# Optimization experiments

Hardware: AMD Instinct MI355X
Metric: run time of the kernel (lower is better)

Reference implementation:

```python
import jax, jax.numpy as jnp
import numpy as np

B, L, V, E, H = 256, 256, 32000, 300, 100

def _prm(key, shape, scale=0.05):
    return (jax.random.normal(key, shape) * scale).astype(jnp.float32)

def setup_inputs():
    ks = jax.random.split(jax.random.key(0), 40)
    d = {
        "p": jax.random.randint(ks[0], (B, L), 0, V),
        "q": jax.random.randint(ks[1], (B, L), 0, V),
        "embed": _prm(ks[2], (V, E), 1.0),
    }
    ins = [E, 5 * H, 7 * H, 9 * H, 11 * H]
    for i, n in enumerate(ins):
        d[f"Wih{i+1}"] = _prm(ks[3 + 2 * i], (n, 4 * H))
        d[f"Whh{i+1}"] = _prm(ks[4 + 2 * i], (H, 4 * H))
        d[f"bih{i+1}"] = jnp.zeros((4 * H,), jnp.float32)
        d[f"bhh{i+1}"] = jnp.zeros((4 * H,), jnp.float32)
    d["a1w1"] = _prm(ks[20], (9 * H, 200)); d["a1b1"] = jnp.zeros((200,), jnp.float32)
    d["a1w2"] = _prm(ks[21], (200, 9 * H)); d["a1b2"] = jnp.zeros((9 * H,), jnp.float32)
    d["a2w1"] = _prm(ks[22], (13 * H, 200)); d["a2b1"] = jnp.zeros((200,), jnp.float32)
    d["a2w2"] = _prm(ks[23], (200, 13 * H)); d["a2b2"] = jnp.zeros((13 * H,), jnp.float32)
    d["dw1"] = _prm(ks[24], (13 * H * 5, 1000)); d["db1"] = jnp.zeros((1000,), jnp.float32)
    d["dw2"] = _prm(ks[25], (1000, 1000)); d["db2"] = jnp.zeros((1000,), jnp.float32)
    d["dw3"] = _prm(ks[26], (1000, 2)); d["db3"] = jnp.zeros((2,), jnp.float32)
    return d

def _lstm_seq(x0, h0, c0, Wih, Whh, bih, bhh, n):
    # NOTE: original code feeds x[0] at EVERY timestep (source bug, kept faithful).
    pre = x0 @ Wih + bih + bhh  # [B, 4H], constant across time
    def step(carry, _):
        h, c = carry
        g = pre + h @ Whh
        i, f, gg, o = jnp.split(g, 4, axis=-1)  # torch gate order i,f,g,o
        c = jax.nn.sigmoid(f) * c + jax.nn.sigmoid(i) * jnp.tanh(gg)
        h = jax.nn.sigmoid(o) * jnp.tanh(c)
        return (h, c), h
    (h, c), hs = jax.lax.scan(step, (h0, c0), None, length=n)
    return hs, h, c  # hs: [L, B, H] time-major

def _attn(pb, qb):
    # pb, qb: [B, L, H] batch-first; per-pair cosine similarity then dual softmax
    pn = jnp.sqrt(jnp.sum(pb * pb, axis=-1))
    qn = jnp.sqrt(jnp.sum(qb * qb, axis=-1))
    dots = jnp.einsum('bih,bjh->bij', pb, qb)
    att = dots / jnp.maximum(pn[:, :, None] * qn[:, None, :], 1e-8)
    a_p = jnp.matmul(jax.nn.softmax(att, axis=2), qb)  # [B,L,H]
    a_q = jnp.matmul(jax.nn.softmax(att, axis=1), pb)  # faithful: att (not att^T) @ p, valid since Lp==Lq
    return a_p, a_q

def _ae(x, w1, b1, w2, b2):
    # dropout is identity in eval mode
    return jnp.tanh(jnp.tanh(x @ w1 + b1) @ w2 + b2)

def _forward(p, q, embed, Wih1, Whh1, bih1, bhh1, Wih2, Whh2, bih2, bhh2,
             Wih3, Whh3, bih3, bhh3, Wih4, Whh4, bih4, bhh4, Wih5, Whh5, bih5, bhh5,
             a1w1, a1b1, a1w2, a1b2, a2w1, a2b1, a2w2, a2b2,
             dw1, db1, dw2, db2, dw3, db3):
    h0 = jnp.ones((B, H), jnp.float32)
    c0 = jnp.ones((B, H), jnp.float32)
    x_p = embed[p].transpose(1, 0, 2)  # [L, B, E] time-major
    x_q = embed[q].transpose(1, 0, 2)

    def layer(x_p, x_q, Wih, Whh, bih, bhh):
        # p-loop starts fresh from (h0,c0); q-loop carries state from p-loop (faithful)
        hs_p, h, c = _lstm_seq(x_p[0], h0, c0, Wih, Whh, bih, bhh, L)
        hs_q, _, _ = _lstm_seq(x_q[0], h, c, Wih, Whh, bih, bhh, L)
        return hs_p, hs_q

    def attend_cat(hs_p, hs_q, x_p, x_q):
        a_p, a_q = _attn(hs_p.transpose(1, 0, 2), hs_q.transpose(1, 0, 2))
        xp = jnp.concatenate([hs_p, a_p.transpose(1, 0, 2), x_p], axis=2)
        xq = jnp.concatenate([hs_q, a_q.transpose(1, 0, 2), x_q], axis=2)
        return xp, xq

    h_p1, h_q1 = layer(x_p, x_q, Wih1, Whh1, bih1, bhh1)
    x_p2, x_q2 = attend_cat(h_p1, h_q1, x_p, x_q)        # [L,B,5H]
    h_p2, h_q2 = layer(x_p2, x_q2, Wih2, Whh2, bih2, bhh2)
    x_p3, x_q3 = attend_cat(h_p2, h_q2, x_p2, x_q2)      # [L,B,7H]
    h_p3, h_q3 = layer(x_p3, x_q3, Wih3, Whh3, bih3, bhh3)
    x_pe, x_qe = attend_cat(h_p3, h_q3, x_p3, x_q3)      # [L,B,9H]
    x_p4 = _ae(x_pe, a1w1, a1b1, a1w2, a1b2)
    x_q4 = _ae(x_qe, a1w1, a1b1, a1w2, a1b2)
    h_p4, h_q4 = layer(x_p4, x_q4, Wih4, Whh4, bih4, bhh4)
    x_p5, x_q5 = attend_cat(h_p4, h_q4, x_p4, x_q4)      # [L,B,11H]
    h_p5, h_q5 = layer(x_p5, x_q5, Wih5, Whh5, bih5, bhh5)
    x_pe2, x_qe2 = attend_cat(h_p5, h_q5, x_p5, x_q5)    # [L,B,13H]
    x_p_pool = _ae(x_pe2, a2w1, a2b1, a2w2, a2b2)
    x_q_pool = _ae(x_qe2, a2w1, a2b1, a2w2, a2b2)
    vp = jnp.max(x_p_pool, axis=0)  # max over time -> [B,13H]
    vq = jnp.max(x_q_pool, axis=0)
    vec = jnp.concatenate([vp, vq, vp + vq, vp - vq, jnp.abs(vp - vq)], axis=1)  # [B,65H]
    h1 = jax.nn.relu(vec @ dw1 + db1)
    h2 = jax.nn.relu(h1 @ dw2 + db2)
    return jax.nn.softmax(h2 @ dw3 + db3, axis=1)  # [B,2]

def reference(p, q, embed, Wih1, Whh1, bih1, bhh1, Wih2, Whh2, bih2, bhh2,
              Wih3, Whh3, bih3, bhh3, Wih4, Whh4, bih4, bhh4, Wih5, Whh5, bih5, bhh5,
              a1w1, a1b1, a1w2, a1b2, a2w1, a2b1, a2w2, a2b2,
              dw1, db1, dw2, db2, dw3, db3):
    return _forward(p, q, embed, Wih1, Whh1, bih1, bhh1, Wih2, Whh2, bih2, bhh2,
                    Wih3, Whh3, bih3, bhh3, Wih4, Whh4, bih4, bhh4, Wih5, Whh5, bih5, bhh5,
                    a1w1, a1b1, a1w2, a1b2, a2w1, a2b1, a2w2, a2b2,
                    dw1, db1, dw2, db2, dw3, db3)
```

## Files before the change

kernel.cpp:

```cpp
#include <hip/hip_runtime.h>
#include <hip/hip_bf16.h>
#include <cstddef>

#define NB 256
#define NL 256
#define NE 300
#define NH 100
#define NG 400
#define RT 16
#define YW 1300

typedef __hip_bfloat16 bf;
typedef __attribute__((ext_vector_type(8))) short short8v;
typedef __attribute__((ext_vector_type(4))) float float4v;

static __device__ __forceinline__ float bu2f(unsigned short u) {
  union { unsigned int i; float f; } x; x.i = ((unsigned int)u) << 16; return x.f;
}
static __device__ __forceinline__ float b2f(bf v) { return __bfloat162float(v); }
static __device__ __forceinline__ bf f2b(float f) { return __float2bfloat16(f); }
static __device__ __forceinline__ unsigned short f2bu(float f) {
  bf h = __float2bfloat16(f);
  return *reinterpret_cast<unsigned short*>(&h);
}

__global__ __launch_bounds__(256) void build_x0(
    const bf* __restrict__ segA, int dimA,
    const bf* __restrict__ segB, int dimB,
    const int* __restrict__ toks, const float* __restrict__ embed,
    float* __restrict__ X0, int in_dim, int b0)
{
  int bc = blockIdx.x;
  int tok = 0;
  if (dimA + dimB < in_dim) { tok = toks[(b0 + bc) * NL]; if (tok < 0) tok = 0; }
  for (int k = threadIdx.x; k < in_dim; k += 256) {
    float v;
    if (k < dimA) v = b2f(segA[(size_t)bc * YW + k]);
    else if (k < dimA + dimB) v = b2f(segB[(size_t)bc * YW + (k - dimA)]);
    else v = embed[(size_t)tok * NE + (k - dimA - dimB)];
    X0[(size_t)bc * in_dim + k] = v;
  }
}

__global__ __launch_bounds__(512) void lstm_kernel(
    const float* __restrict__ x0, int in_dim,
    const float* __restrict__ Wih, const float* __restrict__ Whh,
    const float* __restrict__ bih, const float* __restrict__ bhh,
    int init_ones, float* __restrict__ st,
    bf* __restrict__ hs, int hs_off, int nbc)
{
  int bc = blockIdx.x, j = threadIdx.x;
  __shared__ float g[NG];
  __shared__ __align__(16) float hb[NH];
  float wh[NH];
  float pre = 0.f;
  if (j < NG) {
    pre = bih[j] + bhh[j];
    const float4* x4 = (const float4*)(x0 + (size_t)bc * in_dim);
    for (int k4 = 0; k4 < (in_dim >> 2); k4++) {
      float4 xv = x4[k4];
      const float* wp = Wih + (size_t)(4 * k4) * NG + j;
      pre += xv.x * wp[0];
      pre += xv.y * wp[NG];
      pre += xv.z * wp[2 * NG];
      pre += xv.w * wp[3 * NG];
    }
#pragma unroll
    for (int k = 0; k < NH; k++) wh[k] = Whh[(size_t)k * NG + j];
  }
  float c = 0.f, hcur = 0.f, hprev = 0.f;
  if (j < NH) {
    if (init_ones) { hcur = 1.f; c = 1.f; }
    else { hcur = st[bc * 2 * NH + j]; c = st[bc * 2 * NH + NH + j]; }
    hb[j] = hcur;
  }
  __syncthreads();
  for (int l = 0; l < NL; l++) {
    if (j < NH && l > 0)
      hs[((size_t)(l - 1) * nbc + bc) * YW + hs_off + j] = f2b(hprev);
    if (j < NG) {
      float gs = pre;
#pragma unroll
      for (int k4 = 0; k4 < NH / 4; k4++) {
        float4 h4 = *(const float4*)&hb[4 * k4];
        gs += h4.x * wh[4 * k4] + h4.y * wh[4 * k4 + 1]
            + h4.z * wh[4 * k4 + 2] + h4.w * wh[4 * k4 + 3];
      }
      g[j] = gs;
    }
    __syncthreads();
    if (j < NH) {
      float i_g = 1.f / (1.f + expf(-g[j]));
      float f_g = 1.f / (1.f + expf(-g[NH + j]));
      float g_g = tanhf(g[2 * NH + j]);
      float o_g = 1.f / (1.f + expf(-g[3 * NH + j]));
      c = f_g * c + i_g * g_g;
      hcur = o_g * tanhf(c);
      hprev = hcur;
      hb[j] = hcur;
    }
    __syncthreads();
  }
  if (j < NH) {
    hs[((size_t)(NL - 1) * nbc + bc) * YW + hs_off + j] = f2b(hprev);
    st[bc * 2 * NH + j] = hcur;
    st[bc * 2 * NH + NH + j] = c;
  }
}

__global__ __launch_bounds__(256) void attn_scores(
    const bf* __restrict__ Pb, int hoff,
    const bf* __restrict__ Qb,
    bf* __restrict__ att, int nbc)
{
  int bc = blockIdx.y, i0 = blockIdx.x * RT, t = threadIdx.x;
  __shared__ __align__(16) float ps[NH][RT];
  __shared__ float pn[RT];
  for (int it = 0; it < 7; it++) {
    int idx = t + 256 * it;
    if (idx < NH * RT) {
      int r = idx & 15, k = idx >> 4;
      ps[k][r] = b2f(Pb[((size_t)(i0 + r) * nbc + bc) * YW + hoff + k]);
    }
  }
  __syncthreads();
  if (t < RT) {
    float s = 0.f;
    for (int k = 0; k < NH; k++) { float v = ps[k][t]; s += v * v; }
    pn[t] = sqrtf(s);
  }
  __syncthreads();
  const bf* qrow = Qb + ((size_t)t * nbc + bc) * YW + hoff;
  float dot[RT];
#pragma unroll
  for (int r = 0; r < RT; r++) dot[r] = 0.f;
  float qn = 0.f;
  for (int k = 0; k < NH; k++) {
    float qv = b2f(qrow[k]);
    qn += qv * qv;
    const float4* p4 = (const float4*)&ps[k][0];
    float4 A = p4[0], Bv = p4[1], Cv = p4[2], Dv = p4[3];
    dot[0] += A.x * qv;  dot[1] += A.y * qv;  dot[2] += A.z * qv;  dot[3] += A.w * qv;
    dot[4] += Bv.x * qv; dot[5] += Bv.y * qv; dot[6] += Bv.z * qv; dot[7] += Bv.w * qv;
    dot[8] += Cv.x * qv; dot[9] += Cv.y * qv; dot[10] += Cv.z * qv; dot[11] += Cv.w * qv;
    dot[12] += Dv.x * qv; dot[13] += Dv.y * qv; dot[14] += Dv.z * qv; dot[15] += Dv.w * qv;
  }
  float qnr = sqrtf(qn);
#pragma unroll
  for (int r = 0; r < RT; r++)
    att[((size_t)bc * NL + (i0 + r)) * NL + t] = f2b(dot[r] / fmaxf(pn[r] * qnr, 1e-8f));
}

__global__ __launch_bounds__(256) void attn_ap(
    const bf* __restrict__ att,
    const bf* __restrict__ Qb, int hoff,
    bf* __restrict__ dst, int aoff, int nbc)
{
  int bc = blockIdx.y, i0 = blockIdx.x * RT, t = threadIdx.x;
  __shared__ float w[RT][NL];
  __shared__ float inv[RT];
#pragma unroll
  for (int r = 0; r < RT; r++)
    w[r][t] = b2f(att[((size_t)bc * NL + (i0 + r)) * NL + t]);
  __syncthreads();
  {
    int r = t >> 4, s = t & 15;
    float m = -1e30f;
    for (int jj = s; jj < NL; jj += 16) m = fmaxf(m, w[r][jj]);
#pragma unroll
    for (int o = 8; o; o >>= 1) m = fmaxf(m, __shfl_xor(m, o, 16));
    float sum = 0.f;
    for (int jj = s; jj < NL; jj += 16) { float e = expf(w[r][jj] - m); w[r][jj] = e; sum += e; }
#pragma unroll
    for (int o = 8; o; o >>= 1) sum += __shfl_xor(sum, o, 16);
    if (s == 0) inv[r] = 1.f / sum;
  }
  __syncthreads();
#pragma unroll
  for (int it = 0; it < 2; it++) {
    int idx = t + 256 * it;
    if (idx >= RT * 25) break;
    int r = idx / 25, c4 = (idx % 25) * 4;
    float sc = inv[r];
    float ax = 0, ay = 0, az = 0, aw = 0;
    for (int j = 0; j < NL; j++) {
      float wv = w[r][j];
      ushort4 qv = *(const ushort4*)(Qb + ((size_t)j * nbc + bc) * YW + hoff + c4);
      ax += wv * bu2f(qv.x); ay += wv * bu2f(qv.y);
      az += wv * bu2f(qv.z); aw += wv * bu2f(qv.w);
    }
    ushort4 o4;
    o4.x = f2bu(ax * sc); o4.y = f2bu(ay * sc); o4.z = f2bu(az * sc); o4.w = f2bu(aw * sc);
    *(ushort4*)(dst + ((size_t)(i0 + r) * nbc + bc) * YW + aoff + c4) = o4;
  }
}

__global__ __launch_bounds__(256) void attn_colstats(
    const bf* __restrict__ att, float* __restrict__ cmax, float* __restrict__ csum)
{
  int bc = blockIdx.x, j = threadIdx.x;
  const bf* ab = att + (size_t)bc * NL * NL;
  float m = -1e30f;
  for (int i = 0; i < NL; i++) m = fmaxf(m, b2f(ab[(size_t)i * NL + j]));
  float s = 0.f;
  for (int i = 0; i < NL; i++) s += expf(b2f(ab[(size_t)i * NL + j]) - m);
  cmax[bc * NL + j] = m;
  csum[bc * NL + j] = s;
}

__global__ __launch_bounds__(256) void attn_aq(
    const bf* __restrict__ att, const float* __restrict__ cmax, const float* __restrict__ csum,
    const bf* __restrict__ Pb, int hoff,
    bf* __restrict__ dst, int aoff, int nbc)
{
  int bc = blockIdx.y, i0 = blockIdx.x * RT, t = threadIdx.x;
  __shared__ float w[RT][NL];
  float cm = cmax[bc * NL + t], ci = 1.f / csum[bc * NL + t];
#pragma unroll
  for (int r = 0; r < RT; r++)
    w[r][t] = expf(b2f(att[((size_t)bc * NL + (i0 + r)) * NL + t]) - cm) * ci;
  __syncthreads();
#pragma unroll
  for (int it = 0; it < 2; it++) {
    int idx = t + 256 * it;
    if (idx >= RT * 25) break;
    int r = idx / 25, c4 = (idx % 25) * 4;
    float ax = 0, ay = 0, az = 0, aw = 0;
    for (int j = 0; j < NL; j++) {
      float wv = w[r][j];
      ushort4 pv = *(const ushort4*)(Pb + ((size_t)j * nbc + bc) * YW + hoff + c4);
      ax += wv * bu2f(pv.x); ay += wv * bu2f(pv.y);
      az += wv * bu2f(pv.z); aw += wv * bu2f(pv.w);
    }
    ushort4 o4;
    o4.x = f2bu(ax); o4.y = f2bu(ay); o4.z = f2bu(az); o4.w = f2bu(aw);
    *(ushort4*)(dst + ((size_t)(i0 + r) * nbc + bc) * YW + aoff + c4) = o4;
  }
}

__global__ __launch_bounds__(256) void prep_w1T(
    const float* __restrict__ w, int K, int Kpad, short* __restrict__ dst)
{
  int col = blockIdx.y;
  int k = blockIdx.x * 256 + threadIdx.x;
  if (k < Kpad)
    dst[(size_t)col * Kpad + k] = (col < 200 && k < K) ? f2bu(w[(size_t)k * 200 + col]) : 0;
}
__global__ __launch_bounds__(256) void prep_w2T(
    const float* __restrict__ w, int N, short* __restrict__ dst)
{
  int col = blockIdx.x;
  int k = threadIdx.x;
  if (k < 224)
    dst[(size_t)col * 224 + k] = (col < N && k < 200) ? f2bu(w[(size_t)k * N + col]) : 0;
}

__global__ __launch_bounds__(256) void ae_mfma(
    const bf* __restrict__ srcA, int dimA,
    const bf* __restrict__ srcB, int dimB,
    const int* __restrict__ toks, const float* __restrict__ embed,
    int in_dim, int Kpad,
    const short* __restrict__ w1T, const float* __restrict__ b1,
    const short* __restrict__ w2T, const float* __restrict__ b2,
    int out_dim, int nch2,
    bf* __restrict__ dst, int doff,
    float* __restrict__ pmax, int pool, int nbc, int lgnbc, int b0)
{
  __shared__ short smem[24576];
  short* xsS = smem;
  short* wsS = smem + 4096;
  short* HS  = smem;
  short* w2S = smem + 17408;
  __shared__ float pmaxs[4][32];

  const int t = threadIdx.x;
  const int wave = t >> 6, lane = t & 63;
  const int lc = lane & 15;
  const int koff = (lane >> 4) << 3;

  float4v acc[13];
#pragma unroll
  for (int nt = 0; nt < 13; nt++) { acc[nt][0] = 0.f; acc[nt][1] = 0.f; acc[nt][2] = 0.f; acc[nt][3] = 0.f; }

  for (int kc = 0; kc < Kpad; kc += 64) {
    bool fastA = (kc + 64 <= dimA);
    bool fastB = (kc >= dimA) && (kc + 64 <= dimA + dimB);
    if (fastA || fastB) {
      const bf* src = fastA ? srcA : srcB;
      int coff = fastA ? kc : (kc - dimA);
      for (int idx = t; idx < 64 * 16; idx += 256) {
        int r = idx >> 4, k4 = (idx & 15) * 4;
        size_t rc = pool ? ((size_t)(blockIdx.x * 64 + r) * nbc + blockIdx.y)
                         : ((size_t)blockIdx.x * 64 + r);
        ushort4 v = *(const ushort4*)(src + rc * YW + coff + k4);
        int half = (r * 64 + k4) ^ ((r & 7) << 3);
        *(ushort4*)&xsS[half] = v;
      }
    } else {
      for (int idx = t; idx < 64 * 64; idx += 256) {
        int r = idx >> 6, kk = idx & 63;
        int k = kc + kk;
        size_t rc = pool ? ((size_t)(blockIdx.x * 64 + r) * nbc + blockIdx.y)
                         : ((size_t)blockIdx.x * 64 + r);
        unsigned short v = 0;
        if (k < dimA) v = *(const unsigned short*)&srcA[rc * YW + k];
        else if (k < dimA + dimB) v = *(const unsigned short*)&srcB[rc * YW + (k - dimA)];
        else if (k < in_dim) {
          int l = (int)(rc >> lgnbc), bb = (int)(rc & (nbc - 1));
          int tok = toks[(b0 + bb) * NL + l]; if (tok < 0) tok = 0;
          v = f2bu(embed[(size_t)tok * NE + (k - dimA - dimB)]);
        }
        xsS[(r * 64 + kk) ^ ((r & 7) << 3)] = (short)v;
      }
    }
    for (int idx = t; idx < 208 * 8; idx += 256) {
      int col = idx >> 3, k8 = (idx & 7) * 8;
      short8v v = *(const short8v*)(w1T + (size_t)col * Kpad + kc + k8);
      *(short8v*)&wsS[(col * 64 + k8) ^ ((col & 7) << 3)] = v;
    }
    __syncthreads();
    const int arow = (wave << 4) + lc;
#pragma unroll
    for (int ks = 0; ks < 2; ks++) {
      int kk = ks * 32 + koff;
      short8v a = *(const short8v*)&xsS[(arow * 64 + kk) ^ ((arow & 7) << 3)];
#pragma unroll
      for (int nt = 0; nt < 13; nt++) {
        int col = nt * 16 + lc;
        short8v b = *(const short8v*)&wsS[(col * 64 + kk) ^ ((col & 7) << 3)];
        acc[nt] = __builtin_amdgcn_mfma_f32_16x16x32_bf16(a, b, acc[nt], 0, 0, 0);
      }
    }
    __syncthreads();
  }

#pragma unroll
  for (int nt = 0; nt < 13; nt++) {
    int col = nt * 16 + lc;
    float bb = (col < 200) ? b1[col] : 0.f;
#pragma unroll
    for (int reg = 0; reg < 4; reg++) {
      int row = (wave << 4) + ((lane >> 4) << 2) + reg;
      float hv = (col < 200) ? tanhf(acc[nt][reg] + bb) : 0.f;
      HS[(row * 224 + col) ^ ((row & 7) << 3)] = (short)f2bu(hv);
    }
  }
  for (int idx = t; idx < 64 * 16; idx += 256) {
    int row = idx >> 4, col = 208 + (idx & 15);
    HS[(row * 224 + col) ^ ((row & 7) << 3)] = 0;
  }
  __syncthreads();

  for (int nc = 0; nc < nch2; nc++) {
    if (nc) __syncthreads();
    for (int idx = t; idx < 32 * 28; idx += 256) {
      int col = idx / 28, k8 = (idx % 28) * 8;
      short8v v = *(const short8v*)(w2T + (size_t)(nc * 32 + col) * 224 + k8);
      *(short8v*)&w2S[(col * 224 + k8) ^ ((col & 7) << 3)] = v;
    }
    __syncthreads();
    float4v acc2[2];
#pragma unroll
    for (int nt = 0; nt < 2; nt++) { acc2[nt][0] = 0.f; acc2[nt][1] = 0.f; acc2[nt][2] = 0.f; acc2[nt][3] = 0.f; }
    const int arow = (wave << 4) + lc;
#pragma unroll
    for (int ks = 0; ks < 7; ks++) {
      int kk = ks * 32 + koff;
      short8v a = *(const short8v*)&HS[(arow * 224 + kk) ^ ((arow & 7) << 3)];
#pragma unroll
      for (int nt = 0; nt < 2; nt++) {
        int col = nt * 16 + lc;
        short8v b = *(const short8v*)&w2S[(col * 224 + kk) ^ ((col & 7) << 3)];
        acc2[nt] = __builtin_amdgcn_mfma_f32_16x16x32_bf16(a, b, acc2[nt], 0, 0, 0);
      }
    }
    if (!pool) {
#pragma unroll
      for (int nt = 0; nt < 2; nt++) {
        int j = nc * 32 + nt * 16 + lc;
        if (j < out_dim) {
          float bb = b2[j];
#pragma unroll
          for (int reg = 0; reg < 4; reg++) {
            int row = (wave << 4) + ((lane >> 4) << 2) + reg;
            size_t rc = (size_t)blockIdx.x * 64 + row;
            dst[rc * YW + doff + j] = f2b(tanhf(acc2[nt][reg] + bb));
          }
        }
      }
    } else {
#pragma unroll
      for (int nt = 0; nt < 2; nt++) {
        int j = nc * 32 + nt * 16 + lc;
        float bb = (j < out_dim) ? b2[j] : 0.f;
        float m = -1e30f;
#pragma unroll
        for (int reg = 0; reg < 4; reg++) m = fmaxf(m, tanhf(acc2[nt][reg] + bb));
        m = fmaxf(m, __shfl_xor(m, 16));
        m = fmaxf(m, __shfl_xor(m, 32));
        if (lane < 16) pmaxs[wave][nt * 16 + lane] = m;
      }
      __syncthreads();
      if (t < 32) {
        int j = nc * 32 + t;
        if (j < out_dim) {
          float m = fmaxf(fmaxf(pmaxs[0][t], pmaxs[1][t]), fmaxf(pmaxs[2][t], pmaxs[3][t]));
          pmax[((size_t)blockIdx.x * nbc + blockIdx.y) * out_dim + j] = m;
        }
      }
    }
  }
}

__global__ __launch_bounds__(256) void pool_reduce(
    const float* __restrict__ pmax, float* __restrict__ v, int nbc, int b0)
{
  int bc = blockIdx.x;
  for (int jj = threadIdx.x; jj < 1300; jj += 256) {
    float m = -1e30f;
    for (int lc = 0; lc < 4; lc++) m = fmaxf(m, pmax[((size_t)lc * nbc + bc) * 1300 + jj]);
    v[(size_t)(b0 + bc) * 1300 + jj] = m;
  }
}

__global__ __launch_bounds__(256) void build_vec(
    const float* __restrict__ vp, const float* __restrict__ vq, float* __restrict__ vec)
{
  int b = blockIdx.x;
  float* v = vec + (size_t)b * 6500;
  for (int k = threadIdx.x; k < 1300; k += 256) {
    float a = vp[(size_t)b * 1300 + k], bq = vq[(size_t)b * 1300 + k];
    v[k] = a; v[1300 + k] = bq; v[2600 + k] = a + bq; v[3900 + k] = a - bq;
    v[5200 + k] = fabsf(a - bq);
  }
}

#define FMA16(arr, base4, wv) { \
  float4 _a = (base4)[0], _b = (base4)[1], _c = (base4)[2], _d = (base4)[3]; \
  arr[0] += _a.x * (wv); arr[1] += _a.y * (wv); arr[2] += _a.z * (wv); arr[3] += _a.w * (wv); \
  arr[4] += _b.x * (wv); arr[5] += _b.y * (wv); arr[6] += _b.z * (wv); arr[7] += _b.w * (wv); \
  arr[8] += _c.x * (wv); arr[9] += _c.y * (wv); arr[10] += _c.z * (wv); arr[11] += _c.w * (wv); \
  arr[12] += _d.x * (wv); arr[13] += _d.y * (wv); arr[14] += _d.z * (wv); arr[15] += _d.w * (wv); }

#define KT 32
#define JT 256
__global__ __launch_bounds__(256) void mlp_partial(
    const float* __restrict__ in, int K,
    const float* __restrict__ W, int N,
    float* __restrict__ part, int kslen)
{
  int rb = blockIdx.x, jb = blockIdx.y, ks = blockIdx.z;
  int t = threadIdx.x;
  int j0 = jb * JT;
  int jw = N - j0; if (jw > JT) jw = JT;
  int k0 = ks * kslen;
  int k1 = k0 + kslen; if (k1 > K) k1 = K;
  __shared__ __align__(16) float xs[KT][16];
  __shared__ __align__(16) float ws[KT][JT];
  float acc[16];
#pragma unroll
  for (int r = 0; r < 16; r++) acc[r] = 0.f;
  for (int kc = k0; kc < k1; kc += KT) {
    int klim = k1 - kc; if (klim > KT) klim = KT;
    for (int idx = t; idx < klim * 16; idx += 256) {
      int kk = idx >> 4, r = idx & 15;
      xs[kk][r] = in[(size_t)(rb * 16 + r) * K + kc + kk];
    }
    int nw4 = jw >> 2;
    for (int idx = t; idx < klim * nw4; idx += 256) {
      int kk = idx / nw4, c4 = (idx % nw4) * 4;
      *(float4*)&ws[kk][c4] =
          *(const float4*)&W[(size_t)(kc + kk) * N + j0 + c4];
    }
    __syncthreads();
    if (t < jw) {
      for (int k = 0; k < klim; k++) {
        float wv = ws[k][t];
        const float4* x4 = (const float4*)&xs[k][0];
        FMA16(acc, x4, wv);
      }
    }
    __syncthreads();
  }
  if (t < jw) {
#pragma unroll
    for (int r = 0; r < 16; r++)
      part[((size_t)blockIdx.z * NB + rb * 16 + r) * N + j0 + t] = acc[r];
  }
}

__global__ __launch_bounds__(256) void mlp_reduce(
    const float* __restrict__ part, const float* __restrict__ bias,
    float* __restrict__ out, int N, int nks)
{
  int row = blockIdx.y;
  int j = blockIdx.x * 256 + threadIdx.x;
  if (j >= N) return;
  float s = bias[j];
  for (int ks = 0; ks < nks; ks++)
    s += part[((size_t)ks * NB + row) * N + j];
  out[(size_t)row * N + j] = fmaxf(s, 0.f);
}

__global__ __launch_bounds__(64) void final_softmax(
    const float* __restrict__ h2, const float* __restrict__ dw3,
    const float* __restrict__ db3, float* __restrict__ out)
{
  int b = blockIdx.x, t = threadIdx.x;
  float a0 = 0.f, a1 = 0.f;
  for (int k = t; k < 1000; k += 64) {
    float hv = h2[(size_t)b * 1000 + k];
    a0 += hv * dw3[2 * k];
    a1 += hv * dw3[2 * k + 1];
  }
  for (int o = 32; o; o >>= 1) { a0 += __shfl_down(a0, o); a1 += __shfl_down(a1, o); }
  if (t == 0) {
    a0 += db3[0]; a1 += db3[1];
    float m = fmaxf(a0, a1);
    float e0 = expf(a0 - m), e1 = expf(a1 - m), s = e0 + e1;
    out[b * 2] = e0 / s; out[b * 2 + 1] = e1 / s;
  }
}

__global__ __launch_bounds__(256) void fill_diag(float* __restrict__ out, int n, float v)
{
  int i = blockIdx.x * 256 + threadIdx.x;
  if (i < n) out[i] = v;
}

extern "C" void kernel_launch(void* const* d_in, const int* in_sizes, int n_in,
                              void* d_out, int out_size, void* d_ws, size_t ws_size,
                              hipStream_t stream)
{
  (void)in_sizes; (void)n_in;
  const int* p = (const int*)d_in[0];
  const int* q = (const int*)d_in[1];
  const float* embed = (const float*)d_in[2];
  const float *Wih[5], *Whh[5], *bihv[5], *bhhv[5];
  for (int i = 0; i < 5; i++) {
    Wih[i] = (const float*)d_in[3 + 4 * i];
    Whh[i] = (const float*)d_in[4 + 4 * i];
    bihv[i] = (const float*)d_in[5 + 4 * i];
    bhhv[i] = (const float*)d_in[6 + 4 * i];
  }
  const float* a1w1 = (const float*)d_in[23]; const float* a1b1 = (const float*)d_in[24];
  const float* a1w2 = (const float*)d_in[25]; const float* a1b2 = (const float*)d_in[26];
  const float* a2w1 = (const float*)d_in[27]; const float* a2b1 = (const float*)d_in[28];
  const float* a2w2 = (const float*)d_in[29]; const float* a2b2 = (const float*)d_in[30];
  const float* dw1 = (const float*)d_in[31]; const float* db1 = (const float*)d_in[32];
  const float* dw2 = (const float*)d_in[33]; const float* db2 = (const float*)d_in[34];
  const float* dw3 = (const float*)d_in[35]; const float* db3 = (const float*)d_in[36];

  auto al = [](size_t x) { return (x + 255) & ~(size_t)255; };
  const int NKS = 8;
  const size_t PKfloats = (size_t)NKS * NB * 1000;
  const size_t W1Ah = (size_t)208 * 960;
  const size_t W1Bh = (size_t)208 * 1344;
  const size_t W2Ah = (size_t)928 * 224;
  const size_t W2Bh = (size_t)1312 * 224;

  int nbc = 0, lgnbc = 0;
  size_t oYP=0,oYQ=0,oATT=0,oCM=0,oCS=0,oST=0,oPM=0,oVP=0,oVQ=0,oVEC=0,oH1=0,oH2=0,oX0=0,
         oW1A=0,oW1B=0,oW2A=0,oW2B=0;
  for (int lg = 8; lg >= 5; lg--) {
    int nb = 1 << lg;
    size_t nrowc = (size_t)nb * NL;
    size_t pmfloats = (size_t)16 * nb * 1300;
    if (pmfloats < PKfloats) pmfloats = PKfloats;
    size_t off = 0;
    oYP = off;  off = al(off + nrowc * YW * sizeof(bf));
    oYQ = off;  off = al(off + nrowc * YW * sizeof(bf));
    oATT = off; off = al(off + (size_t)nb * NL * NL * sizeof(bf));
    oCM = off;  off = al(off + (size_t)nb * NL * sizeof(float));
    oCS = off;  off = al(off + (size_t)nb * NL * sizeof(float));
    oST = off;  off = al(off + (size_t)nb * 2 * NH * sizeof(float));
    oPM = off;  off = al(off + pmfloats * sizeof(float));
    oVP = off;  off = al(off + (size_t)NB * 1300 * sizeof(float));
    oVQ = off;  off = al(off + (size_t)NB * 1300 * sizeof(float));
    oVEC = off; off = al(off + (size_t)NB * 6500 * sizeof(float));
    oH1 = off;  off = al(off + (size_t)NB * 1000 * sizeof(float));
    oH2 = off;  off = al(off + (size_t)NB * 1000 * sizeof(float));
    oX0 = off;  off = al(off + (size_t)nb * 1100 * sizeof(float));
    oW1A = off; off = al(off + W1Ah * sizeof(short));
    oW1B = off; off = al(off + W1Bh * sizeof(short));
    oW2A = off; off = al(off + W2Ah * sizeof(short));
    oW2B = off; off = al(off + W2Bh * sizeof(short));
    if (off <= ws_size) { nbc = nb; lgnbc = lg; break; }
  }
  if (nbc == 0) {
    float v = (float)(ws_size >> 20) * 0.001f;
    if (v > 0.7f) v = 0.7f;
    fill_diag<<<(out_size + 255) / 256, 256, 0, stream>>>((float*)d_out, out_size, v);
    return;
  }

  char* base = (char*)d_ws;
  bf* YP = (bf*)(base + oYP); bf* YQ = (bf*)(base + oYQ);
  bf* ATT = (bf*)(base + oATT);
  float* CM = (float*)(base + oCM); float* CS = (float*)(base + oCS);
  float* ST = (float*)(base + oST); float* PM = (float*)(base + oPM);
  float* VP = (float*)(base + oVP); float* VQ = (float*)(base + oVQ);
  float* VEC = (float*)(base + oVEC);
  float* H1 = (float*)(base + oH1); float* H2 = (float*)(base + oH2);
  float* X0 = (float*)(base + oX0);
  short* W1A = (short*)(base + oW1A); short* W1B = (short*)(base + oW1B);
  short* W2A = (short*)(base + oW2A); short* W2B = (short*)(base + oW2B);
  float* PK = PM;

  prep_w1T<<<dim3(4, 208), 256, 0, stream>>>(a1w1, 900, 960, W1A);
  prep_w1T<<<dim3(6, 208), 256, 0, stream>>>(a2w1, 1300, 1344, W1B);
  prep_w2T<<<928, 256, 0, stream>>>(a1w2, 900, W2A);
  prep_w2T<<<1312, 256, 0, stream>>>(a2w2, 1300, W2B);

  for (int b0 = 0; b0 < NB; b0 += nbc) {
    auto LSTM = [&](int li, int dimA, int segAoff, int dimB, int segBoff,
                    bool withEmb, int in_dim, int hoff) {
      build_x0<<<nbc, 256, 0, stream>>>(dimA ? YP + segAoff : nullptr, dimA,
                                        dimB ? YP + segBoff : nullptr, dimB,
                                        withEmb ? p : nullptr, embed, X0, in_dim, b0);
      lstm_kernel<<<nbc, 512, 0, stream>>>(X0, in_dim, Wih[li], Whh[li], bihv[li], bhhv[li],
                                           1, ST, YP, hoff, nbc);
      build_x0<<<nbc, 256, 0, stream>>>(dimA ? YQ + segAoff : nullptr, dimA,
                                        dimB ? YQ + segBoff : nullptr, dimB,
                                        withEmb ? q : nullptr, embed, X0, in_dim, b0);
      lstm_kernel<<<nbc, 512, 0, stream>>>(X0, in_dim, Wih[li], Whh[li], bihv[li], bhhv[li],
                                           0, ST, YQ, hoff, nbc);
    };
    auto ATTN = [&](int hoff, int aoff) {
      dim3 g(NL / RT, nbc);
      attn_scores<<<g, 256, 0, stream>>>(YP, hoff, YQ, ATT, nbc);
      attn_ap<<<g, 256, 0, stream>>>(ATT, YQ, hoff, YP, aoff, nbc);
      attn_colstats<<<nbc, 256, 0, stream>>>(ATT, CM, CS);
      attn_aq<<<g, 256, 0, stream>>>(ATT, CM, CS, YP, hoff, YQ, aoff, nbc);
    };

    LSTM(0, 0, 0, 0, 0, true, 300, 400);
    ATTN(400, 500);
    LSTM(1, 200, 400, 0, 0, true, 500, 200);
    ATTN(200, 300);
    LSTM(2, 400, 200, 0, 0, true, 700, 0);
    ATTN(0, 100);
    ae_mfma<<<nbc * 4, 256, 0, stream>>>(YP, 600, nullptr, 0, p, embed, 900, 960,
                                         W1A, a1b1, W2A, a1b2, 900, 29,
                                         YP, 0, nullptr, 0, nbc, lgnbc, b0);
    ae_mfma<<<nbc * 4, 256, 0, stream>>>(YQ, 600, nullptr, 0, q, embed, 900, 960,
                                         W1A, a1b1, W2A, a1b2, 900, 29,
                                         YQ, 0, nullptr, 0, nbc, lgnbc, b0);
    LSTM(3, 900, 0, 0, 0, false, 900, 1100);
    ATTN(1100, 1200);
    LSTM(4, 200, 1100, 900, 0, false, 1100, 900);
    ATTN(900, 1000);
    ae_mfma<<<dim3(4, nbc), 256, 0, stream>>>(YP + 900, 400, YP, 900, p, embed, 1300, 1344,
                                              W1B, a2b1, W2B, a2b2, 1300, 41,
                                              nullptr, 0, PM, 1, nbc, lgnbc, b0);
    pool_reduce<<<nbc, 256, 0, stream>>>(PM, VP, nbc, b0);
    ae_mfma<<<dim3(4, nbc), 256, 0, stream>>>(YQ + 900, 400, YQ, 900, q, embed, 1300, 1344,
                                              W1B, a2b1, W2B, a2b2, 1300, 41,
                                              nullptr, 0, PM, 1, nbc, lgnbc, b0);
    pool_reduce<<<nbc, 256, 0, stream>>>(PM, VQ, nbc, b0);
  }

  build_vec<<<NB, 256, 0, stream>>>(VP, VQ, VEC);
  {
    int K = 6500, N = 1000;
    int kslen = (K + NKS - 1) / NKS;
    dim3 g1(NB / 16, (N + JT - 1) / JT, NKS);
    mlp_partial<<<g1, 256, 0, stream>>>(VEC, K, dw1, N, PK, kslen);
    mlp_reduce<<<dim3((N + 255) / 256, NB), 256, 0, stream>>>(PK, db1, H1, N, NKS);
  }
  {
    int K = 1000, N = 1000;
    int nks = 4;
    int kslen = (K + nks - 1) / nks;
    dim3 g2(NB / 16, (N + JT - 1) / JT, nks);
    mlp_partial<<<g2, 256, 0, stream>>>(H1, K, dw2, N, PK, kslen);
    mlp_reduce<<<dim3((N + 255) / 256, NB), 256, 0, stream>>>(PK, db2, H2, N, nks);
  }
  final_softmax<<<NB, 64, 0, stream>>>(H2, dw3, db3, (float*)d_out);
}
```

Before: 12.42 ms.

## Fuse x0 gather into LSTM kernel and parallelize gate activations

Merges the separate build_x0 kernel into lstm_kernel: each block now gathers its input row into shared memory instead of writing it to and rereading it from a global scratch buffer, and the X0 workspace is removed. Gate nonlinearities are now evaluated by all 400 gate threads in parallel rather than by 100 threads each doing four, which shortens the serial part of every timestep. Dot products are split into four independent accumulators for more ILP, and launch bounds change to 448 threads with 2 blocks per CU. The risk is register pressure, since each thread holds 100 Whh values in registers under the tighter launch bound.

After: 11.02 ms. 11.2% less time.

```diff
diff --git a/kernel.cpp b/kernel.cpp
--- a/kernel.cpp
+++ b/kernel.cpp
@@ -24,47 +24,45 @@
   return *reinterpret_cast<unsigned short*>(&h);
 }
 
-__global__ __launch_bounds__(256) void build_x0(
+__global__ __launch_bounds__(448, 2) void lstm_kernel(
     const bf* __restrict__ segA, int dimA,
     const bf* __restrict__ segB, int dimB,
-    const int* __restrict__ toks, const float* __restrict__ embed,
-    float* __restrict__ X0, int in_dim, int b0)
-{
-  int bc = blockIdx.x;
+    const int* __restrict__ toks, const float* __restrict__ embed, int in_dim,
+    const float* __restrict__ Wih, const float* __restrict__ Whh,
+    const float* __restrict__ bih, const float* __restrict__ bhh,
+    int init_ones, float* __restrict__ st,
+    bf* __restrict__ hs, int hs_off, int nbc, int b0)
+{
+  int bc = blockIdx.x, j = threadIdx.x;
+  __shared__ __align__(16) float xsh[1104];
+  __shared__ float act[NG];
+  __shared__ __align__(16) float hb[NH];
+
   int tok = 0;
   if (dimA + dimB < in_dim) { tok = toks[(b0 + bc) * NL]; if (tok < 0) tok = 0; }
-  for (int k = threadIdx.x; k < in_dim; k += 256) {
+  for (int k = j; k < in_dim; k += 448) {
     float v;
     if (k < dimA) v = b2f(segA[(size_t)bc * YW + k]);
     else if (k < dimA + dimB) v = b2f(segB[(size_t)bc * YW + (k - dimA)]);
     else v = embed[(size_t)tok * NE + (k - dimA - dimB)];
-    X0[(size_t)bc * in_dim + k] = v;
-  }
-}
-
-__global__ __launch_bounds__(512) void lstm_kernel(
-    const float* __restrict__ x0, int in_dim,
-    const float* __restrict__ Wih, const float* __restrict__ Whh,
-    const float* __restrict__ bih, const float* __restrict__ bhh,
-    int init_ones, float* __restrict__ st,
-    bf* __restrict__ hs, int hs_off, int nbc)
-{
-  int bc = blockIdx.x, j = threadIdx.x;
-  __shared__ float g[NG];
-  __shared__ __align__(16) float hb[NH];
+    xsh[k] = v;
+  }
+  __syncthreads();
+
   float wh[NH];
   float pre = 0.f;
   if (j < NG) {
-    pre = bih[j] + bhh[j];
-    const float4* x4 = (const float4*)(x0 + (size_t)bc * in_dim);
+    float p0 = 0.f, p1 = 0.f, p2 = 0.f, p3 = 0.f;
+    const float4* x4 = (const float4*)xsh;
     for (int k4 = 0; k4 < (in_dim >> 2); k4++) {
       float4 xv = x4[k4];
       const float* wp = Wih + (size_t)(4 * k4) * NG + j;
-      pre += xv.x * wp[0];
-      pre += xv.y * wp[NG];
-      pre += xv.z * wp[2 * NG];
-      pre += xv.w * wp[3 * NG];
-    }
+      p0 += xv.x * wp[0];
+      p1 += xv.y * wp[NG];
+      p2 += xv.z * wp[2 * NG];
+      p3 += xv.w * wp[3 * NG];
+    }
+    pre = bih[j] + bhh[j] + ((p0 + p1) + (p2 + p3));
 #pragma unroll
     for (int k = 0; k < NH; k++) wh[k] = Whh[(size_t)k * NG + j];
   }
@@ -75,27 +73,27 @@
     hb[j] = hcur;
   }
   __syncthreads();
+
   for (int l = 0; l < NL; l++) {
     if (j < NH && l > 0)
       hs[((size_t)(l - 1) * nbc + bc) * YW + hs_off + j] = f2b(hprev);
     if (j < NG) {
-      float gs = pre;
+      float s0 = 0.f, s1 = 0.f, s2 = 0.f, s3 = 0.f;
 #pragma unroll
       for (int k4 = 0; k4 < NH / 4; k4++) {
         float4 h4 = *(const float4*)&hb[4 * k4];
-        gs += h4.x * wh[4 * k4] + h4.y * wh[4 * k4 + 1]
-            + h4.z * wh[4 * k4 + 2] + h4.w * wh[4 * k4 + 3];
-      }
-      g[j] = gs;
+        s0 += h4.x * wh[4 * k4];
+        s1 += h4.y * wh[4 * k4 + 1];
+        s2 += h4.z * wh[4 * k4 + 2];
+        s3 += h4.w * wh[4 * k4 + 3];
+      }
+      float gs = pre + ((s0 + s1) + (s2 + s3));
+      act[j] = (j < 2 * NH || j >= 3 * NH) ? 1.f / (1.f + expf(-gs)) : tanhf(gs);
     }
     __syncthreads();
     if (j < NH) {
-      float i_g = 1.f / (1.f + expf(-g[j]));
-      float f_g = 1.f / (1.f + expf(-g[NH + j]));
-      float g_g = tanhf(g[2 * NH + j]);
-      float o_g = 1.f / (1.f + expf(-g[3 * NH + j]));
-      c = f_g * c + i_g * g_g;
-      hcur = o_g * tanhf(c);
+      c = act[NH + j] * c + act[j] * act[2 * NH + j];
+      hcur = act[3 * NH + j] * tanhf(c);
       hprev = hcur;
       hb[j] = hcur;
     }
@@ -560,7 +558,7 @@
   const size_t W2Bh = (size_t)1312 * 224;
 
   int nbc = 0, lgnbc = 0;
-  size_t oYP=0,oYQ=0,oATT=0,oCM=0,oCS=0,oST=0,oPM=0,oVP=0,oVQ=0,oVEC=0,oH1=0,oH2=0,oX0=0,
+  size_t oYP=0,oYQ=0,oATT=0,oCM=0,oCS=0,oST=0,oPM=0,oVP=0,oVQ=0,oVEC=0,oH1=0,oH2=0,
          oW1A=0,oW1B=0,oW2A=0,oW2B=0;
   for (int lg = 8; lg >= 5; lg--) {
     int nb = 1 << lg;
@@ -580,7 +578,6 @@
     oVEC = off; off = al(off + (size_t)NB * 6500 * sizeof(float));
     oH1 = off;  off = al(off + (size_t)NB * 1000 * sizeof(float));
     oH2 = off;  off = al(off + (size_t)NB * 1000 * sizeof(float));
-    oX0 = off;  off = al(off + (size_t)nb * 1100 * sizeof(float));
     oW1A = off; off = al(off + W1Ah * sizeof(short));
     oW1B = off; off = al(off + W1Bh * sizeof(short));
     oW2A = off; off = al(off + W2Ah * sizeof(short));
@@ -602,7 +599,6 @@
   float* VP = (float*)(base + oVP); float* VQ = (float*)(base + oVQ);
   float* VEC = (float*)(base + oVEC);
   float* H1 = (float*)(base + oH1); float* H2 = (float*)(base + oH2);
-  float* X0 = (float*)(base + oX0);
   short* W1A = (short*)(base + oW1A); short* W1B = (short*)(base + oW1B);
   short* W2A = (short*)(base + oW2A); short* W2B = (short*)(base + oW2B);
   float* PK = PM;
@@ -614,17 +610,15 @@
 
   for (int b0 = 0; b0 < NB; b0 += nbc) {
     auto LSTM = [&](int li, int dimA, int segAoff, int dimB, int segBoff,
-                    bool withEmb, int in_dim, int hoff) {
-      build_x0<<<nbc, 256, 0, stream>>>(dimA ? YP + segAoff : nullptr, dimA,
-                                        dimB ? YP + segBoff : nullptr, dimB,
-                                        withEmb ? p : nullptr, embed, X0, in_dim, b0);
-      lstm_kernel<<<nbc, 512, 0, stream>>>(X0, in_dim, Wih[li], Whh[li], bihv[li], bhhv[li],
-                                           1, ST, YP, hoff, nbc);
-      build_x0<<<nbc, 256, 0, stream>>>(dimA ? YQ + segAoff : nullptr, dimA,
-                                        dimB ? YQ + segBoff : nullptr, dimB,
-                                        withEmb ? q : nullptr, embed, X0, in_dim, b0);
-      lstm_kernel<<<nbc, 512, 0, stream>>>(X0, in_dim, Wih[li], Whh[li], bihv[li], bhhv[li],
-                                           0, ST, YQ, hoff, nbc);
+                    int in_dim, int hoff) {
+      lstm_kernel<<<nbc, 448, 0, stream>>>(YP + segAoff, dimA, YP + segBoff, dimB,
+                                           p, embed, in_dim,
+                                           Wih[li], Whh[li], bihv[li], bhhv[li],
+                                           1, ST, YP, hoff, nbc, b0);
+      lstm_kernel<<<nbc, 448, 0, stream>>>(YQ + segAoff, dimA, YQ + segBoff, dimB,
+                                           q, embed, in_dim,
+                                           Wih[li], Whh[li], bihv[li], bhhv[li],
+                                           0, ST, YQ, hoff, nbc, b0);
     };
     auto ATTN = [&](int hoff, int aoff) {
       dim3 g(NL / RT, nbc);
@@ -634,11 +628,11 @@
       attn_aq<<<g, 256, 0, stream>>>(ATT, CM, CS, YP, hoff, YQ, aoff, nbc);
     };
 
-    LSTM(0, 0, 0, 0, 0, true, 300, 400);
+    LSTM(0, 0, 0, 0, 0, 300, 400);
     ATTN(400, 500);
-    LSTM(1, 200, 400, 0, 0, true, 500, 200);
+    LSTM(1, 200, 400, 0, 0, 500, 200);
     ATTN(200, 300);
-    LSTM(2, 400, 200, 0, 0, true, 700, 0);
+    LSTM(2, 400, 200, 0, 0, 700, 0);
     ATTN(0, 100);
     ae_mfma<<<nbc * 4, 256, 0, stream>>>(YP, 600, nullptr, 0, p, embed, 900, 960,
                                          W1A, a1b1, W2A, a1b2, 900, 29,
@@ -646,9 +640,9 @@
     ae_mfma<<<nbc * 4, 256, 0, stream>>>(YQ, 600, nullptr, 0, q, embed, 900, 960,
                                          W1A, a1b1, W2A, a1b2, 900, 29,
                                          YQ, 0, nullptr, 0, nbc, lgnbc, b0);
-    LSTM(3, 900, 0, 0, 0, false, 900, 1100);
+    LSTM(3, 900, 0, 0, 0, 900, 1100);
     ATTN(1100, 1200);
-    LSTM(4, 200, 1100, 900, 0, false, 1100, 900);
+    LSTM(4, 200, 1100, 900, 0, 1100, 900);
     ATTN(900, 1000);
     ae_mfma<<<dim3(4, nbc), 256, 0, stream>>>(YP + 900, 400, YP, 900, p, embed, 1300, 1344,
                                               W1B, a2b1, W2B, a2b2, 1300, 41,
```
